# Kernel optimization log

Hardware: AMD Instinct MI355X
Metric: run time of the kernel (lower is better)

The kernel has to match this reference:

```python
import jax, jax.numpy as jnp
import numpy as np

N = 131072      # points (rays x samples chunk)
E = 8           # spatial sub-networks (centroids)
DIN = 90        # encoded pos+dir features fed to sub-NeRFs (xyz_real=True -> x[:, 3:])
H = 256         # sub-NeRF hidden width
DOUT = 4        # rgb + sigma
MARGIN = 2.0    # boundary_margin
EPS = 1e-8


def setup_inputs() -> dict:
    key = jax.random.key(0)
    k = jax.random.split(key, 5)
    x_xyz = jax.random.uniform(k[0], (N, 3), dtype=jnp.float32)          # routing coords in [0,1)^3
    x_feat = jax.random.normal(k[1], (N, DIN), dtype=jnp.float32)        # encoded features
    x = jnp.concatenate([x_xyz, x_feat], axis=1)                         # [N, 3+DIN]
    centroids = jax.random.uniform(k[2], (E, 3), dtype=jnp.float32)
    W1 = jax.random.normal(k[3], (E, DIN, H), dtype=jnp.float32) * 0.05
    b1 = jnp.zeros((E, H), dtype=jnp.float32)
    W2 = jax.random.normal(k[4], (E, H, DOUT), dtype=jnp.float32) * 0.05
    b2 = jnp.zeros((E, DOUT), dtype=jnp.float32)
    return {"x": x, "centroids": centroids, "W1": W1, "b1": b1, "W2": W2, "b2": b2}


def reference(x, centroids, W1, b1, W2, b2):
    # --- centroid routing (torch.cdist equivalent) ---
    xyz = x[:, :3]                                                       # [N,3]
    d2 = jnp.sum((xyz[:, None, :] - centroids[None, :, :]) ** 2, axis=-1)
    dist = jnp.sqrt(jnp.maximum(d2, 0.0))                                # [N,E]
    inv = 1.0 / (dist + EPS)
    min_d = jnp.min(dist, axis=1, keepdims=True)                         # [N,1]
    inv = jnp.where(dist > MARGIN * min_d, 0.0, inv)                     # zero far experts
    weights = inv / jnp.sum(inv, axis=-1, keepdims=True)                 # [N,E], rows sum to 1

    # --- per-expert sub-NeRF MLP, weighted combine ---
    # Dense-equivalent of masked gather + weighted scatter-add: experts whose
    # weight is exactly 0 contribute nothing, matching the torch masked path.
    feat = x[:, 3:]                                                      # xyz_real=True -> drop xyz
    h = jax.nn.relu(jnp.einsum('nd,edh->enh', feat, W1) + b1[:, None, :])  # [E,N,H]
    out_e = jnp.einsum('enh,eho->eno', h, W2) + b2[:, None, :]             # [E,N,DOUT]
    return jnp.einsum('eno,ne->no', out_e, weights)                        # [N,DOUT]
```

## Files before the change

kernel.cpp:

```cpp
#include <hip/hip_runtime.h>

#define NPTS 131072
#define NE 8
#define DIN 90
#define NH 256

typedef __attribute__((ext_vector_type(8))) short bf16x8;
typedef __attribute__((ext_vector_type(4))) short bf16x4;
typedef __attribute__((ext_vector_type(4))) float f32x4;
typedef __attribute__((ext_vector_type(2))) float f32x2;
typedef __attribute__((ext_vector_type(4))) unsigned int u32x4;
typedef __attribute__((ext_vector_type(2))) unsigned int u32x2;
typedef __attribute__((ext_vector_type(4), aligned(4))) float f32x4a;
typedef __attribute__((ext_vector_type(2), aligned(4))) float f32x2a;

__device__ __forceinline__ unsigned short f2bf(float f) {
  unsigned int u = __float_as_uint(f);
  u += 0x7fffu + ((u >> 16) & 1u);
  return (unsigned short)(u >> 16);
}

#if defined(__has_builtin) && __has_builtin(__builtin_amdgcn_cvt_pk_bf16_f32)
typedef __attribute__((ext_vector_type(2))) __bf16 bf16x2;
__device__ __forceinline__ unsigned int pkbf(float f0, float f1) {
  bf16x2 r = __builtin_amdgcn_cvt_pk_bf16_f32(f0, f1);
  return __builtin_bit_cast(unsigned int, r);
}
#else
__device__ __forceinline__ unsigned int pkbf(float f0, float f1) {
  unsigned int u0 = __float_as_uint(f0) + 0x7fffu;
  unsigned int u1 = __float_as_uint(f1) + 0x7fffu;
  return __builtin_amdgcn_perm(u1, u0, 0x07060302u);
}
#endif

__device__ __forceinline__ bf16x8 cvt8(f32x4 a, f32x4 b) {
  u32x4 r;
  r[0] = pkbf(a[0], a[1]);
  r[1] = pkbf(a[2], a[3]);
  r[2] = pkbf(b[0], b[1]);
  r[3] = pkbf(b[2], b[3]);
  return __builtin_bit_cast(bf16x8, r);
}

__device__ __forceinline__ f32x4 mfma16(bf16x4 a, bf16x4 b, f32x4 c) {
#if defined(__has_builtin) && __has_builtin(__builtin_amdgcn_mfma_f32_16x16x16bf16_1k)
  return __builtin_amdgcn_mfma_f32_16x16x16bf16_1k(a, b, c, 0, 0, 0);
#else
  f32x4 d = c;
  asm("v_mfma_f32_16x16x16_bf16 %0, %1, %2, %0" : "+v"(d) : "v"(a), "v"(b));
  return d;
#endif
}

__global__ __launch_bounds__(256) void prep(const float* __restrict__ W1,
                                            const float* __restrict__ W2,
                                            unsigned short* __restrict__ W1T,
                                            unsigned short* __restrict__ W2T) {
  const int t = threadIdx.x;
  if (blockIdx.x < 32) {
    const int e = blockIdx.x >> 2;
    const int n0 = (blockIdx.x & 3) * 64;
    __shared__ unsigned int ld[64][49];
    const int nl = t & 63;
    const int kq = t >> 6;
#pragma unroll
    for (int j = 0; j < 12; ++j) {
      const int kp2 = kq + 4 * j;
      const int k0 = 2 * kp2, k1 = k0 + 1;
      unsigned int lo = 0, hi = 0;
      if (k0 < DIN) lo = f2bf(W1[((size_t)e * DIN + k0) * NH + n0 + nl]);
      if (k1 < DIN) hi = f2bf(W1[((size_t)e * DIN + k1) * NH + n0 + nl]);
      ld[nl][kp2] = lo | (hi << 16);
    }
    __syncthreads();
    unsigned int* dst = (unsigned int*)(W1T + (size_t)(e * NH + n0) * 96);
#pragma unroll
    for (int j = 0; j < 12; ++j) {
      const int u = t + 256 * j;
      dst[u] = ld[u / 48][u % 48];
    }
  } else {
    unsigned int* dst = (unsigned int*)W2T;
#pragma unroll 4
    for (int j = 0; j < 64; ++j) {
      const int u = t + 256 * j;
      const int m = u & 7;
      const int o = (u >> 3) & 15;
      const int hb = (u >> 7) & 15;
      const int e = u >> 11;
      unsigned int lo = 0, hi = 0;
      if (o < 4) {
        lo = f2bf(W2[((size_t)e * 256 + hb * 16 + 2 * m) * 4 + o]);
        hi = f2bf(W2[((size_t)e * 256 + hb * 16 + 2 * m + 1) * 4 + o]);
      }
      dst[u] = lo | (hi << 16);
    }
  }
}

__global__ __launch_bounds__(256, 3) void meganerf_main(
    const float* __restrict__ x, const float* __restrict__ cent,
    const float* __restrict__ b1, const float* __restrict__ b2,
    const unsigned short* __restrict__ W1T, const unsigned short* __restrict__ W2T,
    float* __restrict__ out) {
  __shared__ float sOut[4][64][4];
  __shared__ float sW[NE][64];
  __shared__ float sB2[64][4];
  __shared__ float sB1[NE * NH];

  const int t    = threadIdx.x;
  const int lane = t & 63;
  const int wid  = t >> 6;
  const int l15  = lane & 15;
  const int l4   = lane >> 4;
  const int row0 = blockIdx.x * 64;

#pragma unroll
  for (int j = 0; j < 2; ++j)
    *(f32x4*)&sB1[t * 4 + j * 1024] = *(const f32x4a*)&b1[t * 4 + j * 1024];

  bf16x8 bfr[4][3];
#pragma unroll
  for (int nf = 0; nf < 4; ++nf) {
    const float* gr = x + (size_t)(row0 + 16 * nf + l15) * 93 + 3;
    f32x4 v0, v1;
    v0 = *(const f32x4a*)(gr + 8 * l4);
    v1 = *(const f32x4a*)(gr + 8 * l4 + 4);
    bfr[nf][0] = cvt8(v0, v1);
    v0 = *(const f32x4a*)(gr + 32 + 8 * l4);
    v1 = *(const f32x4a*)(gr + 36 + 8 * l4);
    bfr[nf][1] = cvt8(v0, v1);
    if (l4 < 3) {
      v0 = *(const f32x4a*)(gr + 64 + 8 * l4);
      v1 = *(const f32x4a*)(gr + 68 + 8 * l4);
    } else {
      f32x2 tl = *(const f32x2a*)(gr + 88);
      v0[0] = tl[0]; v0[1] = tl[1]; v0[2] = 0.f; v0[3] = 0.f;
      v1[0] = 0.f; v1[1] = 0.f; v1[2] = 0.f; v1[3] = 0.f;
    }
    bfr[nf][2] = cvt8(v0, v1);
  }

  if (t < 64) {
    const float* gx = x + (size_t)(row0 + t) * 93;
    float px = gx[0], py = gx[1], pz = gx[2];
    float dist[NE], inv[NE];
    float mind = 3.4e38f;
#pragma unroll
    for (int e = 0; e < NE; ++e) {
      float dx = px - cent[e * 3 + 0];
      float dy = py - cent[e * 3 + 1];
      float dz = pz - cent[e * 3 + 2];
      float d2 = dx * dx + dy * dy + dz * dz;
      float d = sqrtf(fmaxf(d2, 0.f));
      dist[e] = d;
      inv[e] = 1.f / (d + 1e-8f);
      mind = fminf(mind, d);
    }
    float s = 0.f;
#pragma unroll
    for (int e = 0; e < NE; ++e) {
      if (dist[e] > 2.0f * mind) inv[e] = 0.f;
      s += inv[e];
    }
    float rs = 1.f / s;
    float bb[4] = {0.f, 0.f, 0.f, 0.f};
#pragma unroll
    for (int e = 0; e < NE; ++e) {
      float w = inv[e] * rs;
      sW[e][t] = w;
#pragma unroll
      for (int o = 0; o < 4; ++o) bb[o] += w * b2[e * 4 + o];
    }
#pragma unroll
    for (int o = 0; o < 4; ++o) sB2[t][o] = bb[o];
  }
  __syncthreads();

  bf16x8 w1buf[2][6];
  bf16x4 w2f[2][2];
  float wv[4];

  auto loadW1 = [&](int idx, int buf) {
    const int e = idx >> 1, c = idx & 1;
    const unsigned short* p =
        W1T + (size_t)(e * NH + 128 * c + 32 * wid + l15) * 96 + 8 * l4;
#pragma unroll
    for (int mf = 0; mf < 2; ++mf)
#pragma unroll
      for (int ks = 0; ks < 3; ++ks)
        w1buf[buf][mf * 3 + ks] = *(const bf16x8*)(p + mf * (16 * 96) + 32 * ks);
  };
  auto loadW2 = [&](int idx, int buf) {
    const int e = idx >> 1, c = idx & 1;
    const int hb0 = 8 * c + 2 * wid;
    const unsigned short* p = W2T + ((size_t)(e * 16 + hb0) * 256) + l15 * 16 + l4 * 4;
    w2f[buf][0] = *(const bf16x4*)(p);
    w2f[buf][1] = *(const bf16x4*)(p + 256);
  };

  loadW1(0, 0);
  loadW2(0, 0);

  f32x4 facc[4] = {{0.f, 0.f, 0.f, 0.f}, {0.f, 0.f, 0.f, 0.f},
                   {0.f, 0.f, 0.f, 0.f}, {0.f, 0.f, 0.f, 0.f}};

#pragma unroll 2
  for (int i = 0; i < 16; ++i) {
    const int e = i >> 1, c = i & 1, cur = i & 1, nxt = cur ^ 1;
    const int colbase = 128 * c + 32 * wid;

    f32x4 b1v0 = *(const f32x4*)&sB1[e * NH + colbase + 4 * l4];
    f32x4 b1v1 = *(const f32x4*)&sB1[e * NH + colbase + 16 + 4 * l4];
    if (c == 0) {
#pragma unroll
      for (int nf = 0; nf < 4; ++nf) wv[nf] = sW[e][16 * nf + l15];
    }

    const int ip = (i + 1) & 15;
    loadW1(ip, nxt);
    loadW2(ip, nxt);

#pragma unroll
    for (int mf = 0; mf < 2; ++mf) {
      const f32x4 b1v = (mf == 0) ? b1v0 : b1v1;
      f32x4 acc[4];
#pragma unroll
      for (int nf = 0; nf < 4; ++nf)
        acc[nf] = __builtin_amdgcn_mfma_f32_16x16x32_bf16(
            w1buf[cur][mf * 3 + 0], bfr[nf][0], b1v, 0, 0, 0);
#pragma unroll
      for (int ks = 1; ks < 3; ++ks)
#pragma unroll
        for (int nf = 0; nf < 4; ++nf)
          acc[nf] = __builtin_amdgcn_mfma_f32_16x16x32_bf16(
              w1buf[cur][mf * 3 + ks], bfr[nf][ks], acc[nf], 0, 0, 0);

#pragma unroll
      for (int nf = 0; nf < 4; ++nf) {
        const float w = wv[nf];
        f32x4 a = acc[nf];
        f32x2 p0, p1;
        p0[0] = a[0]; p0[1] = a[1];
        p1[0] = a[2]; p1[1] = a[3];
        const f32x2 z = {0.f, 0.f};
        p0 = __builtin_elementwise_max(p0, z) * w;
        p1 = __builtin_elementwise_max(p1, z) * w;
        u32x2 pk;
        pk[0] = pkbf(p0[0], p0[1]);
        pk[1] = pkbf(p1[0], p1[1]);
        facc[nf] = mfma16(__builtin_bit_cast(bf16x4, pk), w2f[cur][mf], facc[nf]);
      }
    }
  }

  if (l15 < 4) {
#pragma unroll
    for (int nf = 0; nf < 4; ++nf)
#pragma unroll
      for (int r = 0; r < 4; ++r)
        sOut[wid][16 * nf + 4 * l4 + r][l15] = facc[nf][r];
  }
  __syncthreads();
  {
    const int row = t >> 2, o = t & 3;
    float v = sB2[row][o] + sOut[0][row][o] + sOut[1][row][o] +
              sOut[2][row][o] + sOut[3][row][o];
    out[row0 * 4 + t] = v;
  }
}

extern "C" void kernel_launch(void* const* d_in, const int* in_sizes, int n_in,
                              void* d_out, int out_size, void* d_ws, size_t ws_size,
                              hipStream_t stream) {
  const float* x    = (const float*)d_in[0];
  const float* cent = (const float*)d_in[1];
  const float* W1   = (const float*)d_in[2];
  const float* b1   = (const float*)d_in[3];
  const float* W2   = (const float*)d_in[4];
  const float* b2   = (const float*)d_in[5];
  float* out = (float*)d_out;

  unsigned short* W1T = (unsigned short*)d_ws;
  unsigned short* W2T = W1T + NE * NH * 96;

  prep<<<33, 256, 0, stream>>>(W1, W2, W1T, W2T);
  meganerf_main<<<NPTS / 64, 256, 0, stream>>>(x, cent, b1, b2, W1T, W2T, out);
}
```

Baseline: 187.9 us.

## Cut weight register buffering to raise occupancy and parallelize W2 prep

The main kernel stops double-buffering the full W1/W2 fragment set. Only the first W1 half-tile is prefetched for the next iteration, and the second half and the W2 fragments are loaded at the start of the current iteration. This lowers register pressure so launch bounds can ask for 4 waves per SIMD instead of 3, trading load latency hiding for occupancy. The W2 conversion in the prep kernel is also spread across 8 blocks (one per expert) instead of a single block.

```diff
diff --git a/kernel.cpp b/kernel.cpp
--- a/kernel.cpp
+++ b/kernel.cpp
@@ -81,25 +81,26 @@
       dst[u] = ld[u / 48][u % 48];
     }
   } else {
-    unsigned int* dst = (unsigned int*)W2T;
-#pragma unroll 4
-    for (int j = 0; j < 64; ++j) {
+    const int e = blockIdx.x - 32;
+    unsigned int* dst = (unsigned int*)W2T + (size_t)e * 2048;
+    const float* src = W2 + (size_t)e * 1024;
+#pragma unroll
+    for (int j = 0; j < 8; ++j) {
       const int u = t + 256 * j;
       const int m = u & 7;
       const int o = (u >> 3) & 15;
       const int hb = (u >> 7) & 15;
-      const int e = u >> 11;
       unsigned int lo = 0, hi = 0;
       if (o < 4) {
-        lo = f2bf(W2[((size_t)e * 256 + hb * 16 + 2 * m) * 4 + o]);
-        hi = f2bf(W2[((size_t)e * 256 + hb * 16 + 2 * m + 1) * 4 + o]);
+        lo = f2bf(src[(hb * 16 + 2 * m) * 4 + o]);
+        hi = f2bf(src[(hb * 16 + 2 * m + 1) * 4 + o]);
       }
       dst[u] = lo | (hi << 16);
     }
   }
 }
 
-__global__ __launch_bounds__(256, 3) void meganerf_main(
+__global__ __launch_bounds__(256, 4) void meganerf_main(
     const float* __restrict__ x, const float* __restrict__ cent,
     const float* __restrict__ b1, const float* __restrict__ b2,
     const unsigned short* __restrict__ W1T, const unsigned short* __restrict__ W2T,
@@ -178,30 +179,36 @@
   }
   __syncthreads();
 
-  bf16x8 w1buf[2][6];
-  bf16x4 w2f[2][2];
+  bf16x8 w1m0[2][3];
+  bf16x8 w1m1[3];
+  bf16x4 w2f[2];
   float wv[4];
 
-  auto loadW1 = [&](int idx, int buf) {
+  auto loadW1mf0 = [&](int idx, int buf) {
     const int e = idx >> 1, c = idx & 1;
     const unsigned short* p =
         W1T + (size_t)(e * NH + 128 * c + 32 * wid + l15) * 96 + 8 * l4;
 #pragma unroll
-    for (int mf = 0; mf < 2; ++mf)
-#pragma unroll
-      for (int ks = 0; ks < 3; ++ks)
-        w1buf[buf][mf * 3 + ks] = *(const bf16x8*)(p + mf * (16 * 96) + 32 * ks);
+    for (int ks = 0; ks < 3; ++ks)
+      w1m0[buf][ks] = *(const bf16x8*)(p + 32 * ks);
   };
-  auto loadW2 = [&](int idx, int buf) {
+  auto loadW1mf1 = [&](int idx) {
+    const int e = idx >> 1, c = idx & 1;
+    const unsigned short* p =
+        W1T + (size_t)(e * NH + 128 * c + 32 * wid + 16 + l15) * 96 + 8 * l4;
+#pragma unroll
+    for (int ks = 0; ks < 3; ++ks)
+      w1m1[ks] = *(const bf16x8*)(p + 32 * ks);
+  };
+  auto loadW2 = [&](int idx) {
     const int e = idx >> 1, c = idx & 1;
     const int hb0 = 8 * c + 2 * wid;
     const unsigned short* p = W2T + ((size_t)(e * 16 + hb0) * 256) + l15 * 16 + l4 * 4;
-    w2f[buf][0] = *(const bf16x4*)(p);
-    w2f[buf][1] = *(const bf16x4*)(p + 256);
+    w2f[0] = *(const bf16x4*)(p);
+    w2f[1] = *(const bf16x4*)(p + 256);
   };
 
-  loadW1(0, 0);
-  loadW2(0, 0);
+  loadW1mf0(0, 0);
 
   f32x4 facc[4] = {{0.f, 0.f, 0.f, 0.f}, {0.f, 0.f, 0.f, 0.f},
                    {0.f, 0.f, 0.f, 0.f}, {0.f, 0.f, 0.f, 0.f}};
@@ -218,40 +225,63 @@
       for (int nf = 0; nf < 4; ++nf) wv[nf] = sW[e][16 * nf + l15];
     }
 
-    const int ip = (i + 1) & 15;
-    loadW1(ip, nxt);
-    loadW2(ip, nxt);
-
-#pragma unroll
-    for (int mf = 0; mf < 2; ++mf) {
-      const f32x4 b1v = (mf == 0) ? b1v0 : b1v1;
-      f32x4 acc[4];
+    loadW1mf1(i);
+    loadW2(i);
+    loadW1mf0((i + 1) & 15, nxt);
+
+    f32x4 acc[4];
+#pragma unroll
+    for (int nf = 0; nf < 4; ++nf)
+      acc[nf] = __builtin_amdgcn_mfma_f32_16x16x32_bf16(
+          w1m0[cur][0], bfr[nf][0], b1v0, 0, 0, 0);
+#pragma unroll
+    for (int ks = 1; ks < 3; ++ks)
 #pragma unroll
       for (int nf = 0; nf < 4; ++nf)
         acc[nf] = __builtin_amdgcn_mfma_f32_16x16x32_bf16(
-            w1buf[cur][mf * 3 + 0], bfr[nf][0], b1v, 0, 0, 0);
-#pragma unroll
-      for (int ks = 1; ks < 3; ++ks)
-#pragma unroll
-        for (int nf = 0; nf < 4; ++nf)
-          acc[nf] = __builtin_amdgcn_mfma_f32_16x16x32_bf16(
-              w1buf[cur][mf * 3 + ks], bfr[nf][ks], acc[nf], 0, 0, 0);
-
-#pragma unroll
-      for (int nf = 0; nf < 4; ++nf) {
-        const float w = wv[nf];
-        f32x4 a = acc[nf];
-        f32x2 p0, p1;
-        p0[0] = a[0]; p0[1] = a[1];
-        p1[0] = a[2]; p1[1] = a[3];
-        const f32x2 z = {0.f, 0.f};
-        p0 = __builtin_elementwise_max(p0, z) * w;
-        p1 = __builtin_elementwise_max(p1, z) * w;
-        u32x2 pk;
-        pk[0] = pkbf(p0[0], p0[1]);
-        pk[1] = pkbf(p1[0], p1[1]);
-        facc[nf] = mfma16(__builtin_bit_cast(bf16x4, pk), w2f[cur][mf], facc[nf]);
-      }
+            w1m0[cur][ks], bfr[nf][ks], acc[nf], 0, 0, 0);
+
+#pragma unroll
+    for (int nf = 0; nf < 4; ++nf) {
+      const float w = wv[nf];
+      f32x4 a = acc[nf];
+      f32x2 p0, p1;
+      p0[0] = a[0]; p0[1] = a[1];
+      p1[0] = a[2]; p1[1] = a[3];
+      const f32x2 z = {0.f, 0.f};
+      p0 = __builtin_elementwise_max(p0, z) * w;
+      p1 = __builtin_elementwise_max(p1, z) * w;
+      u32x2 pk;
+      pk[0] = pkbf(p0[0], p0[1]);
+      pk[1] = pkbf(p1[0], p1[1]);
+      facc[nf] = mfma16(__builtin_bit_cast(bf16x4, pk), w2f[0], facc[nf]);
+    }
+
+#pragma unroll
+    for (int nf = 0; nf < 4; ++nf)
+      acc[nf] = __builtin_amdgcn_mfma_f32_16x16x32_bf16(
+          w1m1[0], bfr[nf][0], b1v1, 0, 0, 0);
+#pragma unroll
+    for (int ks = 1; ks < 3; ++ks)
+#pragma unroll
+      for (int nf = 0; nf < 4; ++nf)
+        acc[nf] = __builtin_amdgcn_mfma_f32_16x16x32_bf16(
+            w1m1[ks], bfr[nf][ks], acc[nf], 0, 0, 0);
+
+#pragma unroll
+    for (int nf = 0; nf < 4; ++nf) {
+      const float w = wv[nf];
+      f32x4 a = acc[nf];
+      f32x2 p0, p1;
+      p0[0] = a[0]; p0[1] = a[1];
+      p1[0] = a[2]; p1[1] = a[3];
+      const f32x2 z = {0.f, 0.f};
+      p0 = __builtin_elementwise_max(p0, z) * w;
+      p1 = __builtin_elementwise_max(p1, z) * w;
+      u32x2 pk;
+      pk[0] = pkbf(p0[0], p0[1]);
+      pk[1] = pkbf(p1[0], p1[1]);
+      facc[nf] = mfma16(__builtin_bit_cast(bf16x4, pk), w2f[1], facc[nf]);
     }
   }
 
@@ -285,6 +315,6 @@
   unsigned short* W1T = (unsigned short*)d_ws;
   unsigned short* W2T = W1T + NE * NH * 96;
 
-  prep<<<33, 256, 0, stream>>>(W1, W2, W1T, W2T);
+  prep<<<40, 256, 0, stream>>>(W1, W2, W1T, W2T);
   meganerf_main<<<NPTS / 64, 256, 0, stream>>>(x, cent, b1, b2, W1T, W2T, out);
 }
```

Measured after the change: 259.1 us. +37.9%, slower.
